# Performance work log

Hardware: AMD Instinct MI355X
Metric: run time of the kernel (lower is better)

The kernel has to match this reference:

```python
import jax, jax.numpy as jnp
import numpy as np

P_DROP = 0.6  # F.dropout default training=True in the original forward

def setup_inputs() -> dict:
    key = jax.random.key(0)
    k1, k2, k3, k4 = jax.random.split(key, 4)
    B, T, V, F, K, O = 32, 12, 1000, 64, 3, 64
    x = jax.random.normal(k1, (B, T, V, F), dtype=jnp.float32)
    Att = jax.random.uniform(k2, (V, V), dtype=jnp.float32)
    cheb = jax.random.normal(k3, (K, V, V), dtype=jnp.float32)   # Chebyshev polynomials T_k(L)
    Theta = jax.random.normal(k4, (K, F, O), dtype=jnp.float32)  # per-order feature transforms
    return {"x": x, "Att": Att, "cheb": cheb, "Theta": Theta}

def reference(x, Att, cheb, Theta):
    # x: [B,T,V,F]; Att: [V,V]; cheb: [K,V,V]; Theta: [K,F,O]
    B, T, V, F = x.shape
    K = cheb.shape[0]
    keep = 1.0 - P_DROP
    # Original draws a fresh dropout mask per (time_step, k); replicate with a fixed key.
    mask = jax.random.bernoulli(jax.random.key(42), keep, (T, K, V, V))
    TkA = cheb * Att                                   # [K,V,V] attention-weighted polynomial
    M = jnp.where(mask, TkA[None] / keep, 0.0)         # [T,K,V,V] inverted dropout
    # rhs = T_k_with_at @ graph_signal, batched over (b,t,k)
    rhs = jnp.einsum('tkuv,btvf->btkuf', M, x)         # [B,T,K,V,F]
    # sum_k rhs_k @ Theta_k  -> [B,T,V,O]; matches permute(0,3,1,2) of stacked outputs
    out = jnp.einsum('btkuf,kfo->btuo', rhs, Theta)
    return jax.nn.relu(out)
```

## Files before the change

kernel.cpp:

```cpp
#include <hip/hip_runtime.h>
#include <hip/hip_bf16.h>
#include <stdint.h>


typedef __attribute__((ext_vector_type(8))) short short8;
typedef __attribute__((ext_vector_type(4))) float f32x4;

__device__ __forceinline__ ushort f2bf(float f) {
  __hip_bfloat16 h = __float2bfloat16(f);
  return *reinterpret_cast<ushort*>(&h);
}

__device__ __forceinline__ void threefry2x32(uint32_t c0, uint32_t c1,
                                             uint32_t& o0, uint32_t& o1) {
  const uint32_t ks0 = 0u;
  const uint32_t ks1 = 42u;
  const uint32_t ks2 = ks0 ^ ks1 ^ 0x1BD11BDAu;
  uint32_t x0 = c0 + ks0;
  uint32_t x1 = c1 + ks1;
#define TFR(r) { x0 += x1; x1 = (x1 << (r)) | (x1 >> (32 - (r))); x1 ^= x0; }
  TFR(13) TFR(15) TFR(26) TFR(6)
  x0 += ks1; x1 += ks2 + 1u;
  TFR(17) TFR(29) TFR(16) TFR(24)
  x0 += ks2; x1 += ks0 + 2u;
  TFR(13) TFR(15) TFR(26) TFR(6)
  x0 += ks0; x1 += ks1 + 3u;
  TFR(17) TFR(29) TFR(16) TFR(24)
  x0 += ks1; x1 += ks2 + 4u;
  TFR(13) TFR(15) TFR(26) TFR(6)
  x0 += ks2; x1 += ks0 + 5u;
#undef TFR
  o0 = x0; o1 = x1;
}

__global__ void build_m(const float* __restrict__ Att,
                        const float* __restrict__ cheb,
                        ushort* __restrict__ Mws) {
  const uint32_t idx = blockIdx.x * 256u + threadIdx.x;
  const uint32_t vp = idx & 1023u;
  const uint32_t up = (idx >> 10) & 1023u;
  const uint32_t tk = idx >> 20;
  float val = 0.f;
  if ((vp < 1000u) & (up < 1000u)) {
    const uint32_t flat = (tk * 1000u + up) * 1000u + vp;
    uint32_t o0, o1;
    threefry2x32(0u, flat, o0, o1);
    const uint32_t bits = o0 ^ o1;
    const float u = __uint_as_float((bits >> 9) | 0x3f800000u) - 1.0f;
    if (u < 0.4f) {
      val = cheb[(tk % 3u) * 1000000u + up * 1000u + vp] *
            Att[up * 1000u + vp] * 2.5f;
    }
  }
  Mws[idx] = f2bf(val);
}

__global__ void transpose_x(const float* __restrict__ x,
                            ushort* __restrict__ xt) {
  __shared__ float lt[64][65];
  const int vc = blockIdx.x, t = blockIdx.y, b = blockIdx.z;
  const int tid = threadIdx.x;
  const int v0 = vc * 64;
#pragma unroll
  for (int i = 0; i < 4; ++i) {
    const int c = i * 256 + tid;
    const int vi = c >> 4, f4 = c & 15;
    float4 q = make_float4(0.f, 0.f, 0.f, 0.f);
    if (v0 + vi < 1000)
      q = *(const float4*)(x + ((((size_t)b * 12 + t) * 1000 + v0 + vi) << 6) + f4 * 4);
    lt[f4 * 4 + 0][vi] = q.x;
    lt[f4 * 4 + 1][vi] = q.y;
    lt[f4 * 4 + 2][vi] = q.z;
    lt[f4 * 4 + 3][vi] = q.w;
  }
  __syncthreads();
  const int f = tid >> 2, g = tid & 3;
  alignas(16) ushort tmp[16];
#pragma unroll
  for (int j = 0; j < 16; ++j) tmp[j] = f2bf(lt[f][g * 16 + j]);
  const size_t base = ((size_t)(t * 2048 + b * 64 + f)) << 10;
  *(uint4*)(xt + base + v0 + g * 16)     = *(const uint4*)&tmp[0];
  *(uint4*)(xt + base + v0 + g * 16 + 8) = *(const uint4*)&tmp[8];
}

#define LDT 72

#define MFMA(a, b, c) __builtin_amdgcn_mfma_f32_16x16x32_bf16((a), (b), (c), 0, 0, 0)

__global__ __launch_bounds__(512, 1)
void cheb_main(const ushort* __restrict__ Mws, const ushort* __restrict__ xt,
               const float* __restrict__ Theta, float* __restrict__ out) {
  __shared__ __align__(16) ushort smem[32768];
  const int tid = threadIdx.x;
  const int lane = tid & 63;
  const int w = tid >> 6;
  const int wu = w >> 1, wn = w & 1;
  const int quad = lane >> 4, l15 = lane & 15;
  const int nt = blockIdx.x, ut = blockIdx.y, t = blockIdx.z;
  const int u0 = ut * 128, n0 = nt * 128;

  ushort* sA  = smem;
  ushort* sB  = smem + 24576;
  ushort* sP  = smem + w * (32 * LDT);
  ushort* sTh = smem + 24576;

  const int srow = lane >> 3;
  const int gchunk = (lane & 7) ^ srow;
  const int rsw = l15 & 7;

  const size_t mbase = (size_t)(t * 3) << 20;
  const size_t xrow0 = (size_t)(t * 2048 + n0);

  f32x4 pacc[3][2][4];
#pragma unroll
  for (int k = 0; k < 3; ++k)
#pragma unroll
    for (int i = 0; i < 2; ++i)
#pragma unroll
      for (int j = 0; j < 4; ++j) pacc[k][i][j] = f32x4{0.f, 0.f, 0.f, 0.f};

#pragma unroll 1
  for (int vc = 0; vc < 16; ++vc) {
    __syncthreads();
#pragma unroll
    for (int q = 0; q < 8; ++q) {
      const int r = q >> 1, j = q & 1;
      const int rr = 8 * (w * 2 + j) + srow;
      const ushort* src = (r < 3)
          ? Mws + mbase + ((size_t)r << 20) + ((size_t)(u0 + rr) << 10) + vc * 64 + gchunk * 8
          : xt + ((xrow0 + rr) << 10) + vc * 64 + gchunk * 8;
      ushort* dst = (r < 3) ? sA + r * 8192 + (w * 2 + j) * 512 + lane * 8
                            : sB + (w * 2 + j) * 512 + lane * 8;
      *(uint4*)dst = *(const uint4*)src;
    }
    __syncthreads();
    __builtin_amdgcn_s_setprio(1);
#pragma unroll
    for (int ks = 0; ks < 2; ++ks) {
      short8 bv[4];
#pragma unroll
      for (int ni = 0; ni < 4; ++ni) {
        const int row = wn * 64 + ni * 16 + l15;
        bv[ni] = *(const short8*)&sB[row * 64 + (((ks * 4 + quad) ^ rsw) * 8)];
      }
#pragma unroll
      for (int k = 0; k < 3; ++k) {
        short8 av[2];
#pragma unroll
        for (int mi = 0; mi < 2; ++mi) {
          const int row = wu * 32 + mi * 16 + l15;
          av[mi] = *(const short8*)&sA[k * 8192 + row * 64 + (((ks * 4 + quad) ^ rsw) * 8)];
        }
#pragma unroll
        for (int mi = 0; mi < 2; ++mi)
#pragma unroll
          for (int ni = 0; ni < 4; ++ni)
            pacc[k][mi][ni] = MFMA(av[mi], bv[ni], pacc[k][mi][ni]);
      }
    }
    __builtin_amdgcn_s_setprio(0);
  }

  f32x4 oacc[2][4];
#pragma unroll
  for (int i = 0; i < 2; ++i)
#pragma unroll
    for (int j = 0; j < 4; ++j) oacc[i][j] = f32x4{0.f, 0.f, 0.f, 0.f};

#pragma unroll
  for (int k = 0; k < 3; ++k) {
    __syncthreads();
#pragma unroll
    for (int mi = 0; mi < 2; ++mi)
#pragma unroll
      for (int ni = 0; ni < 4; ++ni)
#pragma unroll
        for (int r = 0; r < 4; ++r)
          sP[(mi * 16 + quad * 4 + r) * LDT + ni * 16 + l15] = f2bf(pacc[k][mi][ni][r]);
    for (int e = tid; e < 4096; e += 512) {
      const int f = e >> 6, o = e & 63;
      sTh[o * LDT + f] = f2bf(Theta[k * 4096 + e]);
    }
    __syncthreads();
#pragma unroll
    for (int ks = 0; ks < 2; ++ks) {
      short8 a2[2], b2[4];
#pragma unroll
      for (int mi = 0; mi < 2; ++mi)
        a2[mi] = *(const short8*)&sP[(mi * 16 + l15) * LDT + ks * 32 + quad * 8];
#pragma unroll
      for (int ni = 0; ni < 4; ++ni)
        b2[ni] = *(const short8*)&sTh[(ni * 16 + l15) * LDT + ks * 32 + quad * 8];
#pragma unroll
      for (int mi = 0; mi < 2; ++mi)
#pragma unroll
        for (int ni = 0; ni < 4; ++ni)
          oacc[mi][ni] = MFMA(a2[mi], b2[ni], oacc[mi][ni]);
    }
  }

#pragma unroll
  for (int mi = 0; mi < 2; ++mi) {
    const int u_base = u0 + wu * 32 + mi * 16 + quad * 4;
#pragma unroll
    for (int ni = 0; ni < 4; ++ni) {
      const int n = n0 + wn * 64 + ni * 16 + l15;
      const int b = n >> 6, oo = n & 63;
      float* op = out + (((size_t)b * 12 + t) * 1000) * 64 + oo;
#pragma unroll
      for (int r = 0; r < 4; ++r) {
        const int u = u_base + r;
        if (u < 1000) op[(size_t)u * 64] = fmaxf(oacc[mi][ni][r], 0.f);
      }
    }
  }
}

extern "C" void kernel_launch(void* const* d_in, const int* in_sizes, int n_in,
                              void* d_out, int out_size, void* d_ws, size_t ws_size,
                              hipStream_t stream) {
  const float* x     = (const float*)d_in[0];
  const float* Att   = (const float*)d_in[1];
  const float* cheb  = (const float*)d_in[2];
  const float* Theta = (const float*)d_in[3];
  float* out = (float*)d_out;

  ushort* Mws = (ushort*)d_ws;
  ushort* xtw = Mws + 37748736ull;

  build_m<<<147456, 256, 0, stream>>>(Att, cheb, Mws);
  transpose_x<<<dim3(16, 12, 32), 256, 0, stream>>>(x, xtw);
  cheb_main<<<dim3(16, 8, 12), 512, 0, stream>>>(Mws, xtw, Theta, out);
}
```

Baseline: 332.2 us.

## Double-buffer LDS tiles with register prefetch in cheb_main main loop

The K loop is restructured so global loads for the next chunk go into registers while the MFMA burst runs on the current shared-memory buffer. Two ping-pong LDS buffers replace the single one, so only one barrier per chunk is needed. This hides global-load latency behind the matrix multiplies. The change also raises the launch-bounds occupancy hint to 2 blocks. That hint caps registers, and with the large accumulator array plus 16 prefetch vectors it risks spilling, while the doubled LDS footprint may still limit residency to one block per CU.

```diff
diff --git a/kernel.cpp b/kernel.cpp
--- a/kernel.cpp
+++ b/kernel.cpp
@@ -87,10 +87,64 @@
 
 #define MFMA(a, b, c) __builtin_amdgcn_mfma_f32_16x16x32_bf16((a), (b), (c), 0, 0, 0)
 
-__global__ __launch_bounds__(512, 1)
+#define STAGE_LOAD(P0, P1, P2, P3, P4, P5, P6, P7, CO)                        \
+  do {                                                                        \
+    P0 = *(const uint4*)(Mws + ga0 + (CO));                                   \
+    P1 = *(const uint4*)(Mws + ga1 + (CO));                                   \
+    P2 = *(const uint4*)(Mws + ga0 + 1048576 + (CO));                         \
+    P3 = *(const uint4*)(Mws + ga1 + 1048576 + (CO));                         \
+    P4 = *(const uint4*)(Mws + ga0 + 2097152 + (CO));                         \
+    P5 = *(const uint4*)(Mws + ga1 + 2097152 + (CO));                         \
+    P6 = *(const uint4*)(xt + gx0 + (CO));                                    \
+    P7 = *(const uint4*)(xt + gx1 + (CO));                                    \
+  } while (0)
+
+#define STAGE_WRITE(P0, P1, P2, P3, P4, P5, P6, P7, BP)                       \
+  do {                                                                        \
+    *(uint4*)&(BP)[da0]         = P0;                                         \
+    *(uint4*)&(BP)[da1]         = P1;                                         \
+    *(uint4*)&(BP)[8192 + da0]  = P2;                                         \
+    *(uint4*)&(BP)[8192 + da1]  = P3;                                         \
+    *(uint4*)&(BP)[16384 + da0] = P4;                                         \
+    *(uint4*)&(BP)[16384 + da1] = P5;                                         \
+    *(uint4*)&(BP)[24576 + da0] = P6;                                         \
+    *(uint4*)&(BP)[24576 + da1] = P7;                                         \
+  } while (0)
+
+#define BURST(BP)                                                             \
+  do {                                                                        \
+    const ushort* sAc = (BP);                                                 \
+    const ushort* sBc = (BP) + 24576;                                         \
+    _Pragma("unroll")                                                         \
+    for (int ks = 0; ks < 2; ++ks) {                                          \
+      short8 bv[4];                                                           \
+      _Pragma("unroll")                                                       \
+      for (int ni = 0; ni < 4; ++ni) {                                        \
+        const int row = wn * 64 + ni * 16 + l15;                              \
+        bv[ni] = *(const short8*)&sBc[row * 64 + (((ks * 4 + quad) ^ rsw) * 8)]; \
+      }                                                                       \
+      _Pragma("unroll")                                                       \
+      for (int k = 0; k < 3; ++k) {                                           \
+        short8 av[2];                                                         \
+        _Pragma("unroll")                                                     \
+        for (int mi = 0; mi < 2; ++mi) {                                      \
+          const int row = wu * 32 + mi * 16 + l15;                            \
+          av[mi] = *(const short8*)&sAc[k * 8192 + row * 64 +                 \
+                                        (((ks * 4 + quad) ^ rsw) * 8)];       \
+        }                                                                     \
+        _Pragma("unroll")                                                     \
+        for (int mi = 0; mi < 2; ++mi)                                        \
+          _Pragma("unroll")                                                   \
+          for (int ni = 0; ni < 4; ++ni)                                      \
+            pacc[k][mi][ni] = MFMA(av[mi], bv[ni], pacc[k][mi][ni]);          \
+      }                                                                       \
+    }                                                                         \
+  } while (0)
+
+__global__ __launch_bounds__(512, 2)
 void cheb_main(const ushort* __restrict__ Mws, const ushort* __restrict__ xt,
                const float* __restrict__ Theta, float* __restrict__ out) {
-  __shared__ __align__(16) ushort smem[32768];
+  __shared__ __align__(16) ushort smem[65536];
   const int tid = threadIdx.x;
   const int lane = tid & 63;
   const int w = tid >> 6;
@@ -99,8 +153,8 @@
   const int nt = blockIdx.x, ut = blockIdx.y, t = blockIdx.z;
   const int u0 = ut * 128, n0 = nt * 128;
 
-  ushort* sA  = smem;
-  ushort* sB  = smem + 24576;
+  ushort* buf0 = smem;
+  ushort* buf1 = smem + 32768;
   ushort* sP  = smem + w * (32 * LDT);
   ushort* sTh = smem + 24576;
 
@@ -111,6 +165,15 @@
   const size_t mbase = (size_t)(t * 3) << 20;
   const size_t xrow0 = (size_t)(t * 2048 + n0);
 
+  const int rr0 = 8 * (w * 2 + 0) + srow;
+  const int rr1 = 8 * (w * 2 + 1) + srow;
+  const size_t ga0 = mbase + ((size_t)(u0 + rr0) << 10) + gchunk * 8;
+  const size_t ga1 = mbase + ((size_t)(u0 + rr1) << 10) + gchunk * 8;
+  const size_t gx0 = ((xrow0 + rr0) << 10) + gchunk * 8;
+  const size_t gx1 = ((xrow0 + rr1) << 10) + gchunk * 8;
+  const int da0 = (w * 2 + 0) * 512 + lane * 8;
+  const int da1 = (w * 2 + 1) * 512 + lane * 8;
+
   f32x4 pacc[3][2][4];
 #pragma unroll
   for (int k = 0; k < 3; ++k)
@@ -119,46 +182,29 @@
 #pragma unroll
       for (int j = 0; j < 4; ++j) pacc[k][i][j] = f32x4{0.f, 0.f, 0.f, 0.f};
 
+  uint4 p0, p1, p2, p3, p4, p5, p6, p7;
+  uint4 q0, q1, q2, q3, q4, q5, q6, q7;
+
+  STAGE_LOAD(q0, q1, q2, q3, q4, q5, q6, q7, 0);
+  STAGE_LOAD(p0, p1, p2, p3, p4, p5, p6, p7, 64);
+  STAGE_WRITE(q0, q1, q2, q3, q4, q5, q6, q7, buf0);
+  __syncthreads();
+
 #pragma unroll 1
-  for (int vc = 0; vc < 16; ++vc) {
-    __syncthreads();
-#pragma unroll
-    for (int q = 0; q < 8; ++q) {
-      const int r = q >> 1, j = q & 1;
-      const int rr = 8 * (w * 2 + j) + srow;
-      const ushort* src = (r < 3)
-          ? Mws + mbase + ((size_t)r << 20) + ((size_t)(u0 + rr) << 10) + vc * 64 + gchunk * 8
-          : xt + ((xrow0 + rr) << 10) + vc * 64 + gchunk * 8;
-      ushort* dst = (r < 3) ? sA + r * 8192 + (w * 2 + j) * 512 + lane * 8
-                            : sB + (w * 2 + j) * 512 + lane * 8;
-      *(uint4*)dst = *(const uint4*)src;
-    }
-    __syncthreads();
+  for (int it = 0; it < 8; ++it) {
+    const int vc = it * 2;
     __builtin_amdgcn_s_setprio(1);
-#pragma unroll
-    for (int ks = 0; ks < 2; ++ks) {
-      short8 bv[4];
-#pragma unroll
-      for (int ni = 0; ni < 4; ++ni) {
-        const int row = wn * 64 + ni * 16 + l15;
-        bv[ni] = *(const short8*)&sB[row * 64 + (((ks * 4 + quad) ^ rsw) * 8)];
-      }
-#pragma unroll
-      for (int k = 0; k < 3; ++k) {
-        short8 av[2];
-#pragma unroll
-        for (int mi = 0; mi < 2; ++mi) {
-          const int row = wu * 32 + mi * 16 + l15;
-          av[mi] = *(const short8*)&sA[k * 8192 + row * 64 + (((ks * 4 + quad) ^ rsw) * 8)];
-        }
-#pragma unroll
-        for (int mi = 0; mi < 2; ++mi)
-#pragma unroll
-          for (int ni = 0; ni < 4; ++ni)
-            pacc[k][mi][ni] = MFMA(av[mi], bv[ni], pacc[k][mi][ni]);
-      }
-    }
+    BURST(buf0);
     __builtin_amdgcn_s_setprio(0);
+    if (vc < 15) STAGE_WRITE(p0, p1, p2, p3, p4, p5, p6, p7, buf1);
+    if (vc < 14) STAGE_LOAD(q0, q1, q2, q3, q4, q5, q6, q7, (size_t)(vc + 2) * 64);
+    __syncthreads();
+    __builtin_amdgcn_s_setprio(1);
+    BURST(buf1);
+    __builtin_amdgcn_s_setprio(0);
+    if (vc + 1 < 15) STAGE_WRITE(q0, q1, q2, q3, q4, q5, q6, q7, buf0);
+    if (vc + 1 < 14) STAGE_LOAD(p0, p1, p2, p3, p4, p5, p6, p7, (size_t)(vc + 3) * 64);
+    __syncthreads();
   }
 
   f32x4 oacc[2][4];
```

New measurement: 286.9 us. -13.6%, faster.

## Prepack operands in MFMA fragment order and load directly to registers

Applied to the files above, without the earlier changes.

The dropout matrix and transposed x are now written in a layout that matches the MFMA fragment order, so the main kernel loads A/B operands straight from global memory into registers without staging through shared memory or barriers. The block shrinks to 256 threads with a 64-row u tile, allowing two blocks per CU, and a swizzled 1D grid groups blocks for L2 reuse. This removes LDS traffic and syncs in the main loop, at the cost of no data sharing across waves within a block, so more global/L2 reads.

```diff
diff --git a/kernel.cpp b/kernel.cpp
--- a/kernel.cpp
+++ b/kernel.cpp
@@ -35,11 +35,16 @@
 
 __global__ void build_m(const float* __restrict__ Att,
                         const float* __restrict__ cheb,
-                        ushort* __restrict__ Mws) {
+                        ushort* __restrict__ Mf) {
   const uint32_t idx = blockIdx.x * 256u + threadIdx.x;
-  const uint32_t vp = idx & 1023u;
-  const uint32_t up = (idx >> 10) & 1023u;
+  const uint32_t j = idx & 7u;
+  const uint32_t lane = (idx >> 3) & 63u;
+  const uint32_t ks = (idx >> 9) & 1u;
+  const uint32_t c = (idx >> 10) & 15u;
+  const uint32_t u16 = (idx >> 14) & 63u;
   const uint32_t tk = idx >> 20;
+  const uint32_t up = u16 * 16u + (lane & 15u);
+  const uint32_t vp = c * 64u + ks * 32u + (lane >> 4) * 8u + j;
   float val = 0.f;
   if ((vp < 1000u) & (up < 1000u)) {
     const uint32_t flat = (tk * 1000u + up) * 1000u + vp;
@@ -52,11 +57,11 @@
             Att[up * 1000u + vp] * 2.5f;
     }
   }
-  Mws[idx] = f2bf(val);
+  Mf[idx] = f2bf(val);
 }
 
 __global__ void transpose_x(const float* __restrict__ x,
-                            ushort* __restrict__ xt) {
+                            ushort* __restrict__ xtf) {
   __shared__ float lt[64][65];
   const int vc = blockIdx.x, t = blockIdx.y, b = blockIdx.z;
   const int tid = threadIdx.x;
@@ -78,38 +83,47 @@
   alignas(16) ushort tmp[16];
 #pragma unroll
   for (int j = 0; j < 16; ++j) tmp[j] = f2bf(lt[f][g * 16 + j]);
-  const size_t base = ((size_t)(t * 2048 + b * 64 + f)) << 10;
-  *(uint4*)(xt + base + v0 + g * 16)     = *(const uint4*)&tmp[0];
-  *(uint4*)(xt + base + v0 + g * 16 + 8) = *(const uint4*)&tmp[8];
+  const int n16 = b * 4 + (f >> 4);
+  const int ks = g >> 1;
+  const int l0 = (f & 15) + 16 * ((g & 1) * 2);
+  const size_t fb = ((((size_t)(t * 128 + n16) * 16 + vc) * 2 + ks) << 9);
+  *(uint4*)(xtf + fb + (size_t)l0 * 8)        = *(const uint4*)&tmp[0];
+  *(uint4*)(xtf + fb + (size_t)(l0 + 16) * 8) = *(const uint4*)&tmp[8];
 }
 
 #define LDT 72
-
 #define MFMA(a, b, c) __builtin_amdgcn_mfma_f32_16x16x32_bf16((a), (b), (c), 0, 0, 0)
 
-__global__ __launch_bounds__(512, 1)
-void cheb_main(const ushort* __restrict__ Mws, const ushort* __restrict__ xt,
+__global__ __launch_bounds__(256, 2)
+void cheb_main(const ushort* __restrict__ Mf, const ushort* __restrict__ xtf,
                const float* __restrict__ Theta, float* __restrict__ out) {
-  __shared__ __align__(16) ushort smem[32768];
+  __shared__ __align__(16) ushort smem[13824];
   const int tid = threadIdx.x;
   const int lane = tid & 63;
   const int w = tid >> 6;
   const int wu = w >> 1, wn = w & 1;
   const int quad = lane >> 4, l15 = lane & 15;
-  const int nt = blockIdx.x, ut = blockIdx.y, t = blockIdx.z;
-  const int u0 = ut * 128, n0 = nt * 128;
-
-  ushort* sA  = smem;
-  ushort* sB  = smem + 24576;
-  ushort* sP  = smem + w * (32 * LDT);
-  ushort* sTh = smem + 24576;
-
-  const int srow = lane >> 3;
-  const int gchunk = (lane & 7) ^ srow;
-  const int rsw = l15 & 7;
-
-  const size_t mbase = (size_t)(t * 3) << 20;
-  const size_t xrow0 = (size_t)(t * 2048 + n0);
+
+  const int bid = blockIdx.x;
+  const int swz = (bid & 7) * 384 + (bid >> 3);
+  const int nt = swz & 15;
+  const int g = swz >> 4;
+  const int ut = g & 15;
+  const int t = g >> 4;
+  const int u0 = ut * 64, n0 = nt * 128;
+
+  size_t fA[3][2];
+#pragma unroll
+  for (int k = 0; k < 3; ++k)
+#pragma unroll
+    for (int mi = 0; mi < 2; ++mi)
+      fA[k][mi] = (((size_t)((t * 3 + k) * 64 + ut * 4 + wu * 2 + mi)) << 14)
+                  + (size_t)lane * 8;
+  size_t fB[4];
+#pragma unroll
+  for (int ni = 0; ni < 4; ++ni)
+    fB[ni] = (((size_t)(t * 128 + nt * 8 + wn * 4 + ni)) << 14)
+             + (size_t)lane * 8;
 
   f32x4 pacc[3][2][4];
 #pragma unroll
@@ -121,46 +135,35 @@
 
 #pragma unroll 1
   for (int vc = 0; vc < 16; ++vc) {
-    __syncthreads();
-#pragma unroll
-    for (int q = 0; q < 8; ++q) {
-      const int r = q >> 1, j = q & 1;
-      const int rr = 8 * (w * 2 + j) + srow;
-      const ushort* src = (r < 3)
-          ? Mws + mbase + ((size_t)r << 20) + ((size_t)(u0 + rr) << 10) + vc * 64 + gchunk * 8
-          : xt + ((xrow0 + rr) << 10) + vc * 64 + gchunk * 8;
-      ushort* dst = (r < 3) ? sA + r * 8192 + (w * 2 + j) * 512 + lane * 8
-                            : sB + (w * 2 + j) * 512 + lane * 8;
-      *(uint4*)dst = *(const uint4*)src;
-    }
-    __syncthreads();
+    const size_t co = (size_t)vc << 10;
+    short8 a[3][2][2], b[4][2];
+#pragma unroll
+    for (int ni = 0; ni < 4; ++ni)
+#pragma unroll
+      for (int ks = 0; ks < 2; ++ks)
+        b[ni][ks] = *(const short8*)(xtf + fB[ni] + co + ((size_t)ks << 9));
+#pragma unroll
+    for (int k = 0; k < 3; ++k)
+#pragma unroll
+      for (int mi = 0; mi < 2; ++mi)
+#pragma unroll
+        for (int ks = 0; ks < 2; ++ks)
+          a[k][mi][ks] = *(const short8*)(Mf + fA[k][mi] + co + ((size_t)ks << 9));
     __builtin_amdgcn_s_setprio(1);
 #pragma unroll
-    for (int ks = 0; ks < 2; ++ks) {
-      short8 bv[4];
-#pragma unroll
-      for (int ni = 0; ni < 4; ++ni) {
-        const int row = wn * 64 + ni * 16 + l15;
-        bv[ni] = *(const short8*)&sB[row * 64 + (((ks * 4 + quad) ^ rsw) * 8)];
-      }
-#pragma unroll
-      for (int k = 0; k < 3; ++k) {
-        short8 av[2];
-#pragma unroll
-        for (int mi = 0; mi < 2; ++mi) {
-          const int row = wu * 32 + mi * 16 + l15;
-          av[mi] = *(const short8*)&sA[k * 8192 + row * 64 + (((ks * 4 + quad) ^ rsw) * 8)];
-        }
+    for (int ks = 0; ks < 2; ++ks)
+#pragma unroll
+      for (int k = 0; k < 3; ++k)
 #pragma unroll
         for (int mi = 0; mi < 2; ++mi)
 #pragma unroll
           for (int ni = 0; ni < 4; ++ni)
-            pacc[k][mi][ni] = MFMA(av[mi], bv[ni], pacc[k][mi][ni]);
-      }
-    }
+            pacc[k][mi][ni] = MFMA(a[k][mi][ks], b[ni][ks], pacc[k][mi][ni]);
     __builtin_amdgcn_s_setprio(0);
   }
 
+  ushort* sP  = smem + w * 2304;
+  ushort* sTh = smem + 9216;
   f32x4 oacc[2][4];
 #pragma unroll
   for (int i = 0; i < 2; ++i)
@@ -177,7 +180,7 @@
 #pragma unroll
         for (int r = 0; r < 4; ++r)
           sP[(mi * 16 + quad * 4 + r) * LDT + ni * 16 + l15] = f2bf(pacc[k][mi][ni][r]);
-    for (int e = tid; e < 4096; e += 512) {
+    for (int e = tid; e < 4096; e += 256) {
       const int f = e >> 6, o = e & 63;
       sTh[o * LDT + f] = f2bf(Theta[k * 4096 + e]);
     }
@@ -225,10 +228,10 @@
   const float* Theta = (const float*)d_in[3];
   float* out = (float*)d_out;
 
-  ushort* Mws = (ushort*)d_ws;
-  ushort* xtw = Mws + 37748736ull;
-
-  build_m<<<147456, 256, 0, stream>>>(Att, cheb, Mws);
-  transpose_x<<<dim3(16, 12, 32), 256, 0, stream>>>(x, xtw);
-  cheb_main<<<dim3(16, 8, 12), 512, 0, stream>>>(Mws, xtw, Theta, out);
-}
+  ushort* Mf  = (ushort*)d_ws;
+  ushort* xtf = Mf + 37748736ull;
+
+  build_m<<<147456, 256, 0, stream>>>(Att, cheb, Mf);
+  transpose_x<<<dim3(16, 12, 32), 256, 0, stream>>>(x, xtf);
+  cheb_main<<<3072, 256, 0, stream>>>(Mf, xtf, Theta, out);
+}
```

New measurement: 284.9 us. 1.17x faster.
